# Performance work log

Measured on AMD Instinct MI355X. Metric: run time of the kernel, lower is better.

Reference implementation:

```python
import jax, jax.numpy as jnp
import numpy as np

NUM_HEADS = 8

def _ln(x, w, b, eps=1e-5):
    m = x.mean(-1, keepdims=True)
    v = ((x - m) ** 2).mean(-1, keepdims=True)
    return (x - m) / jnp.sqrt(v + eps) * w + b

def _conv3(x, w, b):
    y = jax.lax.conv_general_dilated(x, w, (1, 1), 'SAME',
                                     dimension_numbers=('NCHW', 'OIHW', 'NCHW'))
    return y + b[None, :, None, None]

def _pos_encoding(c, h, w, dtype):
    # first c//2 channels: x position in [0,1]; next c//2: y position
    px = jnp.broadcast_to(jnp.linspace(0, 1, w, dtype=dtype)[None, :], (h, w))
    py = jnp.broadcast_to(jnp.linspace(0, 1, h, dtype=dtype)[:, None], (h, w))
    pe = jnp.concatenate([jnp.broadcast_to(px, (c // 2, h, w)),
                          jnp.broadcast_to(py, (c // 2, h, w))], axis=0)
    return pe[None]  # [1,c,h,w]

def _pixel_shuffle(x, r=2):
    b, c4, h, w = x.shape
    c = c4 // (r * r)
    return x.reshape(b, c, r, r, h, w).transpose(0, 1, 4, 2, 5, 3).reshape(b, c, h * r, w * r)

def _forward(x, text_hidden, proj_w, proj_b, cf_w, cf_b,
             blk_qw, blk_qb, blk_kw, blk_kb, blk_vw, blk_vb,
             blk_ow, blk_ob, blk_ln1w, blk_ln1b, blk_ln2w, blk_ln2b,
             up_w, up_b, cl_w, cl_b):
    B = x.shape[0]
    # text projection: [B, L, text_dim] -> [B, L, C]
    tf = jnp.einsum('bld,cd->blc', text_hidden, proj_w) + proj_b
    feat = _conv3(x, cf_w, cf_b)  # [B, C, H, W]
    _, C, H, W = feat.shape
    L = tf.shape[1]
    hd = C // NUM_HEADS
    scale = hd ** (-0.5)
    pe = _pos_encoding(C, H, W, feat.dtype)

    def block(feat, p):
        qw, qb, kw, kb, vw, vb, ow, ob, l1w, l1b, l2w, l2b = p
        q = jnp.einsum('oi,bihw->bohw', qw, feat) + qb[None, :, None, None]
        q = q + pe * 0.05
        q_flat = q.reshape(B, C, H * W).transpose(0, 2, 1)  # [B, HW, C]
        q_norm = _ln(q_flat, l1w, l1b)
        qh = q_norm.reshape(B, H * W, NUM_HEADS, hd).transpose(0, 2, 1, 3)
        k = jnp.einsum('blc,oc->blo', tf, kw) + kb
        v = jnp.einsum('blc,oc->blo', tf, vw) + vb
        kn = _ln(k, l2w, l2b)
        kh = kn.reshape(B, L, NUM_HEADS, hd).transpose(0, 2, 1, 3)
        vh = v.reshape(B, L, NUM_HEADS, hd).transpose(0, 2, 1, 3)
        attn = jax.nn.softmax(jnp.einsum('bhnd,bhld->bhnl', qh, kh) * scale, axis=-1)
        out = jnp.einsum('bhnl,bhld->bhnd', attn, vh)          # [B, H8, HW, hd]
        out = out.transpose(0, 2, 1, 3).reshape(B, H * W, C)   # [B, HW, C]
        out = out.transpose(0, 2, 1).reshape(B, C, H, W)
        out = jnp.einsum('oi,bihw->bohw', ow, out) + ob[None, :, None, None]
        return out + feat, None

    blk_params = (blk_qw, blk_qb, blk_kw, blk_kb, blk_vw, blk_vb,
                  blk_ow, blk_ob, blk_ln1w, blk_ln1b, blk_ln2w, blk_ln2b)
    feat, _ = jax.lax.scan(block, feat, blk_params)

    for i in range(up_w.shape[0]):
        feat = jax.nn.relu(_pixel_shuffle(_conv3(feat, up_w[i], up_b[i]), 2))
    return _conv3(feat, cl_w, cl_b)


def setup_inputs() -> dict:
    key = jax.random.key(0)
    ks = jax.random.split(key, 20)
    B, H, W = 8, 64, 64
    C, D, L, NB = 64, 512, 77, 16
    s = 0.05
    inp = {
        'x': jax.random.normal(ks[0], (B, 3, H, W), jnp.float32),
        'text_hidden': jax.random.normal(ks[1], (B, L, D), jnp.float32),
        'proj_w': jax.random.normal(ks[2], (C, D), jnp.float32) * 0.01,
        'proj_b': jnp.zeros((C,), jnp.float32),
        'cf_w': jax.random.normal(ks[3], (C, 3, 3, 3), jnp.float32) * s,
        'cf_b': jnp.zeros((C,), jnp.float32),
        'blk_qw': jax.random.normal(ks[4], (NB, C, C), jnp.float32) * s,
        'blk_qb': jnp.zeros((NB, C), jnp.float32),
        'blk_kw': jax.random.normal(ks[5], (NB, C, C), jnp.float32) * 0.01,
        'blk_kb': jnp.zeros((NB, C), jnp.float32),
        'blk_vw': jax.random.normal(ks[6], (NB, C, C), jnp.float32) * 0.01,
        'blk_vb': jnp.zeros((NB, C), jnp.float32),
        'blk_ow': jax.random.normal(ks[7], (NB, C, C), jnp.float32) * s,
        'blk_ob': jnp.zeros((NB, C), jnp.float32),
        'blk_ln1w': jnp.ones((NB, C), jnp.float32),
        'blk_ln1b': jnp.zeros((NB, C), jnp.float32),
        'blk_ln2w': jnp.ones((NB, C), jnp.float32),
        'blk_ln2b': jnp.zeros((NB, C), jnp.float32),
        'up_w': jax.random.normal(ks[8], (2, C * 4, C, 3, 3), jnp.float32) * s,
        'up_b': jnp.zeros((2, C * 4), jnp.float32),
        'cl_w': jax.random.normal(ks[9], (3, C, 3, 3), jnp.float32) * s,
        'cl_b': jnp.zeros((3,), jnp.float32),
    }
    return inp


def reference(x, text_hidden, proj_w, proj_b, cf_w, cf_b,
              blk_qw, blk_qb, blk_kw, blk_kb, blk_vw, blk_vb,
              blk_ow, blk_ob, blk_ln1w, blk_ln1b, blk_ln2w, blk_ln2b,
              up_w, up_b, cl_w, cl_b):
    return _forward(x, text_hidden, proj_w, proj_b, cf_w, cf_b,
                    blk_qw, blk_qb, blk_kw, blk_kb, blk_vw, blk_vb,
                    blk_ow, blk_ob, blk_ln1w, blk_ln1b, blk_ln2w, blk_ln2b,
                    up_w, up_b, cl_w, cl_b)
```

## Files before the change

### kernel.cpp

```cpp
#include <hip/hip_runtime.h>
#include <math.h>

#define BATCH 8
#define C 64
#define NH 8
#define HD 8
#define LTXT 77
#define H0 64
#define W0 64
#define HW0 (H0*W0)

typedef __attribute__((ext_vector_type(8))) short bfrag;
typedef __attribute__((ext_vector_type(4))) float ffrag;
typedef __attribute__((ext_vector_type(8))) unsigned short us8;
typedef __attribute__((ext_vector_type(4))) unsigned short us4;
typedef __attribute__((ext_vector_type(2))) float f2;

#if defined(__has_builtin)
#if __has_builtin(__builtin_amdgcn_exp2f)
#define EXP2(x) __builtin_amdgcn_exp2f(x)
#else
#define EXP2(x) exp2f(x)
#endif
#else
#define EXP2(x) exp2f(x)
#endif

__device__ __forceinline__ unsigned short f2bf(float f) {
    unsigned u = __builtin_bit_cast(unsigned, f);
    u += 0x7fff + ((u >> 16) & 1);
    return (unsigned short)(u >> 16);
}

__global__ void text_proj_kernel(const float* __restrict__ th, const float* __restrict__ pw,
                                 const float* __restrict__ pb, float* __restrict__ tf) {
    __shared__ float sh[512];
    int bl = blockIdx.x;
    int c = threadIdx.x;
    const float* row = th + (size_t)bl * 512;
    for (int i = c; i < 512; i += 64) sh[i] = row[i];
    __syncthreads();
    const float* wrow = pw + c * 512;
    float acc = pb[c];
    for (int i = 0; i < 512; i += 4) {
        acc += sh[i] * wrow[i] + sh[i+1] * wrow[i+1] + sh[i+2] * wrow[i+2] + sh[i+3] * wrow[i+3];
    }
    tf[bl * 64 + c] = acc;
}

__global__ void __launch_bounds__(256)
prep_kernel(const float* __restrict__ x, const float* __restrict__ cf_w,
            const float* __restrict__ cf_b, float* __restrict__ feat,
            const float* __restrict__ up_w,
            unsigned short* __restrict__ PW1, unsigned short* __restrict__ PW2,
            const float* __restrict__ cl_w, unsigned short* __restrict__ PWF,
            const float* __restrict__ qw, const float* __restrict__ ow,
            unsigned short* __restrict__ PQ, unsigned short* __restrict__ PO) {
    int blk = blockIdx.x;
    if (blk < 8192) {
        int idx = blk * 256 + threadIdx.x;
        int wx = idx & 63;
        int h = (idx >> 6) & 63;
        int o = (idx >> 12) & 63;
        int b = idx >> 18;
        const float* wr = cf_w + o * 27;
        float acc = cf_b[o];
        for (int ci = 0; ci < 3; ci++) {
            for (int ky = 0; ky < 3; ky++) {
                int y = h + ky - 1;
                if ((unsigned)y >= 64u) continue;
                const float* xr = x + (((size_t)b * 3 + ci) * 64 + y) * 64;
                const float* wk = wr + ci * 9 + ky * 3;
                if (wx > 0) acc += xr[wx - 1] * wk[0];
                acc += xr[wx] * wk[1];
                if (wx < 63) acc += xr[wx + 1] * wk[2];
            }
        }
        feat[idx] = acc;
    } else if (blk < 8192 + 1152) {
        int e0 = blk - 8192;
        int st = e0 / 576;
        int e = (e0 % 576) * 256 + threadIdx.x;
        const float* w = up_w + (size_t)st * 147456;
        unsigned short* d = st ? PW2 : PW1;
        int j = e & 7, n = (e >> 3) & 255, q = (e >> 11) & 3, s = (e >> 13) & 1, t = e >> 14;
        int c = n & 63, g = n >> 6;
        int co = 4 * c + g, ci = 32 * s + 8 * q + j;
        d[e] = f2bf(w[co * 576 + ci * 9 + t]);
    } else if (blk < 8192 + 1152 + 36) {
        int e = (blk - 8192 - 1152) * 256 + threadIdx.x;
        int j = e & 7, n = (e >> 3) & 15, q = (e >> 7) & 3, s = (e >> 9) & 1, t = e >> 10;
        int ci = 32 * s + 8 * q + j;
        float v = (n < 3) ? cl_w[n * 576 + ci * 9 + t] : 0.f;
        PWF[e] = f2bf(v);
    } else {
        int e = (blk - 8192 - 1152 - 36) * 256 + threadIdx.x;
        int j = e & 7, n = (e >> 3) & 63, quad = (e >> 9) & 3, kt = (e >> 11) & 1, layer = e >> 12;
        int c = kt * 32 + quad * 8 + j;
        PQ[e] = f2bf(qw[layer * 4096 + n * 64 + c]);
        PO[e] = f2bf(ow[layer * 4096 + n * 64 + c]);
    }
}

__global__ void kv_all_kernel(const float* __restrict__ tf,
                              const float* __restrict__ kw, const float* __restrict__ kb,
                              const float* __restrict__ vw, const float* __restrict__ vb,
                              const float* __restrict__ l2w, const float* __restrict__ l2b,
                              float* __restrict__ kvbuf) {
    __shared__ float sh[64];
    int g = blockIdx.x;
    int bl = g % (BATCH * LTXT);
    int blk = g / (BATCH * LTXT);
    int o = threadIdx.x;
    sh[o] = tf[bl * 64 + o];
    __syncthreads();
    const float* kr = kw + blk * 4096 + o * 64;
    const float* vr = vw + blk * 4096 + o * 64;
    float ka = kb[blk * 64 + o], va = vb[blk * 64 + o];
    for (int c2 = 0; c2 < 64; c2++) {
        float t = sh[c2];
        ka += t * kr[c2];
        va += t * vr[c2];
    }
    float s = ka;
    for (int off = 32; off; off >>= 1) s += __shfl_xor(s, off, 64);
    float mean = s * (1.0f / 64.0f);
    float d = ka - mean;
    float s2 = d * d;
    for (int off = 32; off; off >>= 1) s2 += __shfl_xor(s2, off, 64);
    float rstd = rsqrtf(s2 * (1.0f / 64.0f) + 1e-5f);
    float kn = (d * rstd * l2w[blk * 64 + o] + l2b[blk * 64 + o]) * 0.51006973f;
    size_t base = ((size_t)blk * (BATCH * LTXT) + bl) * 128;
    int hd = o >> 3, ch = o & 7;
    kvbuf[base + hd * 16 + ch]     = kn;
    kvbuf[base + hd * 16 + 8 + ch] = va;
}

__global__ void __launch_bounds__(1024, 8)
attn_all_kernel(const float* __restrict__ feat,
                const float* __restrict__ kvbuf,
                const unsigned short* __restrict__ PQ, const unsigned short* __restrict__ PO,
                const float* __restrict__ qb_a, const float* __restrict__ ob_a,
                const float* __restrict__ l1w_a, const float* __restrict__ l1b_a,
                unsigned short* __restrict__ X1) {
    __shared__ __attribute__((aligned(16))) unsigned short sfb[64][72];
    __shared__ __attribute__((aligned(16))) unsigned short sob[64][72];
    __shared__ __attribute__((aligned(16))) float qf[64][68];
    __shared__ float so[64][64];
    __shared__ __attribute__((aligned(16))) float red[2][4][64];
    __shared__ float ss1[8][64];

    int b = blockIdx.x >> 6;
    int tile = blockIdx.x & 63;
    int n0 = tile << 6;
    int wv = __builtin_amdgcn_readfirstlane(threadIdx.x >> 6);
    int lane = threadIdx.x & 63;
    int p = lane;
    int quad = lane >> 4, n16 = lane & 15;
    int mt = wv >> 2, nt = wv & 3;
    int o0 = wv * 4;
    int h = wv >> 1, half = wv & 1;
    int a0 = h * 8;
    const float* fbase = feat + ((size_t)b << 18) + n0;

    float rres[4];
#pragma unroll
    for (int j = 0; j < 4; j++) rres[j] = fbase[(o0 + j) * HW0 + p];
    {
        us4 v;
#pragma unroll
        for (int j = 0; j < 4; j++) v[j] = f2bf(rres[j]);
        *(us4*)&sfb[p][o0] = v;
    }

    const float pxk = 0.05f / 63.0f;
    float py005 = (float)tile * pxk;
    __syncthreads();

#pragma unroll 1
    for (int layer = 0; layer < 16; layer++) {
        const float* qb = qb_a + layer * 64;
        const float* ob = ob_a + layer * 64;
        const float* l1w = l1w_a + layer * 64;
        const float* l1b = l1b_a + layer * 64;

        {
            bfrag af0 = *(const bfrag*)&sfb[mt * 16 + n16][quad * 8];
            bfrag af1 = *(const bfrag*)&sfb[mt * 16 + n16][32 + quad * 8];
            const unsigned short* bq = PQ + layer * 4096 + (size_t)((quad * 64) + nt * 16 + n16) * 8;
            bfrag bf0 = *(const bfrag*)bq;
            bfrag bf1 = *(const bfrag*)(bq + 2048);
            ffrag cc = (ffrag)0.f;
            cc = __builtin_amdgcn_mfma_f32_16x16x32_bf16(af0, bf0, cc, 0, 0, 0);
            cc = __builtin_amdgcn_mfma_f32_16x16x32_bf16(af1, bf1, cc, 0, 0, 0);
            int cch = nt * 16 + n16;
            float qbv = qb[cch];
            int p0 = mt * 16 + quad * 4;
            float pe0 = (nt < 2) ? (float)p0 * pxk : py005;
            float ped = (nt < 2) ? pxk : 0.f;
            float ov[4];
            ov[0] = cc[0] + qbv + pe0;
            ov[1] = cc[1] + qbv + pe0 + ped;
            ov[2] = cc[2] + qbv + pe0 + 2.f * ped;
            ov[3] = cc[3] + qbv + pe0 + 3.f * ped;
            float4 o4 = {ov[0], ov[1], ov[2], ov[3]};
            *(float4*)&qf[cch][p0] = o4;

            float sv[4], sq[4];
#pragma unroll
            for (int r = 0; r < 4; r++) {
                float s = ov[r], s2v = ov[r] * ov[r];
                s += __shfl_xor(s, 1);  s2v += __shfl_xor(s2v, 1);
                s += __shfl_xor(s, 2);  s2v += __shfl_xor(s2v, 2);
                s += __shfl_xor(s, 4);  s2v += __shfl_xor(s2v, 4);
                s += __shfl_xor(s, 8);  s2v += __shfl_xor(s2v, 8);
                sv[r] = s; sq[r] = s2v;
            }
            if (n16 == 0) {
                *(float4*)&red[0][nt][p0] = (float4){sv[0], sv[1], sv[2], sv[3]};
                *(float4*)&red[1][nt][p0] = (float4){sq[0], sq[1], sq[2], sq[3]};
            }
        }
        __syncthreads();

        {
            float ts = red[0][0][p] + red[0][1][p] + red[0][2][p] + red[0][3][p];
            float ts2 = red[1][0][p] + red[1][1][p] + red[1][2][p] + red[1][3][p];
            float mean = ts * (1.0f / 64.0f);
            float var = ts2 * (1.0f / 64.0f) - mean * mean;
            float rstd = rsqrtf(var + 1e-5f);

            f2 qv[4];
#pragma unroll
            for (int j = 0; j < 4; j++) {
                float qa  = (qf[a0 + 2 * j][p]     - mean) * rstd * l1w[a0 + 2 * j]     + l1b[a0 + 2 * j];
                float qbv = (qf[a0 + 2 * j + 1][p] - mean) * rstd * l1w[a0 + 2 * j + 1] + l1b[a0 + 2 * j + 1];
                qv[j][0] = qa;
                qv[j][1] = qbv;
            }
            const float* kvb = kvbuf + ((size_t)layer * BATCH * LTXT + (size_t)b * LTXT) * 128 + h * 16;
            int l0 = half ? 39 : 0;
            int l1 = half ? 77 : 39;
            float ssum = 0.f;
            f2 acc2[4] = {(f2)0.f, (f2)0.f, (f2)0.f, (f2)0.f};
            for (int l = l0; l < l1; l++) {
                const float4* r = (const float4*)(kvb + (size_t)l * 128);
                float4 k0 = r[0], k1 = r[1];
                f2 d2 = qv[0] * (f2){k0.x, k0.y};
                d2 += qv[1] * (f2){k0.z, k0.w};
                d2 += qv[2] * (f2){k1.x, k1.y};
                d2 += qv[3] * (f2){k1.z, k1.w};
                float e = EXP2(d2[0] + d2[1]);
                ssum += e;
                float4 v0 = r[2], v1 = r[3];
                f2 e2 = {e, e};
                acc2[0] += e2 * (f2){v0.x, v0.y};
                acc2[1] += e2 * (f2){v0.z, v0.w};
                acc2[2] += e2 * (f2){v1.x, v1.y};
                acc2[3] += e2 * (f2){v1.z, v1.w};
            }
            if (half) {
#pragma unroll
                for (int j = 0; j < 4; j++) {
                    so[a0 + 2 * j][p] = acc2[j][0];
                    so[a0 + 2 * j + 1][p] = acc2[j][1];
                }
                ss1[h][p] = ssum;
            }
            __syncthreads();
            if (!half) {
                float inv = 1.0f / (ssum + ss1[h][p]);
                us8 v;
#pragma unroll
                for (int j = 0; j < 4; j++) {
                    v[2*j]   = f2bf((acc2[j][0] + so[a0 + 2*j][p]) * inv);
                    v[2*j+1] = f2bf((acc2[j][1] + so[a0 + 2*j+1][p]) * inv);
                }
                *(us8*)&sob[p][a0] = v;
            }
        }
        __syncthreads();

        {
            bfrag af0 = *(const bfrag*)&sob[mt * 16 + n16][quad * 8];
            bfrag af1 = *(const bfrag*)&sob[mt * 16 + n16][32 + quad * 8];
            const unsigned short* bo = PO + layer * 4096 + (size_t)((quad * 64) + nt * 16 + n16) * 8;
            bfrag bf0 = *(const bfrag*)bo;
            bfrag bf1 = *(const bfrag*)(bo + 2048);
            ffrag cc = (ffrag)0.f;
            cc = __builtin_amdgcn_mfma_f32_16x16x32_bf16(af0, bf0, cc, 0, 0, 0);
            cc = __builtin_amdgcn_mfma_f32_16x16x32_bf16(af1, bf1, cc, 0, 0, 0);
            int cch = nt * 16 + n16;
            float obv = ob[cch];
            int p0 = mt * 16 + quad * 4;
            float4 o4;
            o4.x = cc[0] + obv; o4.y = cc[1] + obv; o4.z = cc[2] + obv; o4.w = cc[3] + obv;
            *(float4*)&qf[cch][p0] = o4;
        }
        __syncthreads();

        {
            us4 v;
#pragma unroll
            for (int j = 0; j < 4; j++) {
                rres[j] += qf[o0 + j][p];
                v[j] = f2bf(rres[j]);
            }
            *(us4*)&sfb[p][o0] = v;
        }
        __syncthreads();
    }

    us4 v;
#pragma unroll
    for (int j = 0; j < 4; j++) v[j] = f2bf(rres[j]);
    *(us4*)(X1 + ((size_t)(b * 4096 + n0 + p)) * 64 + o0) = v;
}

__global__ void __launch_bounds__(256)
upconv_mfma_kernel(const unsigned short* __restrict__ X, const unsigned short* __restrict__ Bp,
                   const float* __restrict__ bias, unsigned short* __restrict__ Y,
                   int Hin, int Win) {
    __shared__ __attribute__((aligned(16))) unsigned short sx[3 * 66 * 72];

    int y = blockIdx.y;
    int wv = threadIdx.x >> 6;
    int lane = threadIdx.x & 63;
    int q = lane >> 4, n16 = lane & 15;
    int m0 = blockIdx.x * 64;
    int hw = Hin * Win;
    int b = m0 / hw, rem = m0 % hw;
    int h = rem / Win, w0 = rem % Win;
    const unsigned short* Xb = X + (size_t)b * hw * 64;

    const us8 z8 = (us8)(unsigned short)0;
    for (int e = threadIdx.x; e < 1584; e += 256) {
        int ch8 = e & 7;
        int pxi = (e >> 3) % 66;
        int row = e / 528;
        int hh = h + row - 1, wp = w0 + pxi - 1;
        us8 v = z8;
        if ((unsigned)hh < (unsigned)Hin && (unsigned)wp < (unsigned)Win)
            v = *(const us8*)(Xb + ((size_t)hh * Win + wp) * 64 + ch8 * 8);
        *(us8*)&sx[row * 4752 + pxi * 72 + ch8 * 8] = v;
    }
    __syncthreads();

    ffrag acc[4][2];
#pragma unroll
    for (int i = 0; i < 4; i++)
#pragma unroll
        for (int j2 = 0; j2 < 2; j2++) acc[i][j2] = (ffrag)0.f;

    int npb = y * 128 + wv * 32;

    for (int t = 0; t < 9; t++) {
        int dy = t / 3, dx = t % 3;
        bfrag af[4][2];
#pragma unroll
        for (int mt = 0; mt < 4; mt++) {
            const unsigned short* sp = &sx[dy * 4752 + (mt * 16 + n16 + dx) * 72 + q * 8];
            af[mt][0] = *(const bfrag*)sp;
            af[mt][1] = *(const bfrag*)(sp + 32);
        }
#pragma unroll
        for (int s = 0; s < 2; s++) {
#pragma unroll
            for (int nt = 0; nt < 2; nt++) {
                bfrag bf = *(const bfrag*)(Bp + (size_t)((((t * 2 + s) * 4 + q) * 256) + npb + nt * 16 + n16) * 8);
#pragma unroll
                for (int mt = 0; mt < 4; mt++)
                    acc[mt][nt] = __builtin_amdgcn_mfma_f32_16x16x32_bf16(af[mt][s], bf, acc[mt][nt], 0, 0, 0);
            }
        }
    }

    int g = y * 2 + (wv >> 1);
    int r1 = y, r2 = wv >> 1;
    int cbase = (wv & 1) * 32;
    float bv[2];
#pragma unroll
    for (int nt = 0; nt < 2; nt++) bv[nt] = bias[4 * (cbase + nt * 16 + n16) + g];
    int Wo = Win * 2;
    unsigned short* Yb = Y + ((size_t)b * Hin * 2 * Wo + (size_t)(2 * h + r1) * Wo + r2) * 64;
#pragma unroll
    for (int mt = 0; mt < 4; mt++) {
#pragma unroll
        for (int r = 0; r < 4; r++) {
            int m = mt * 16 + q * 4 + r;
            unsigned short* dst = Yb + (size_t)(2 * (w0 + m)) * 64;
#pragma unroll
            for (int nt = 0; nt < 2; nt++) {
                float v = acc[mt][nt][r] + bv[nt];
                v = fmaxf(v, 0.f);
                dst[cbase + nt * 16 + n16] = f2bf(v);
            }
        }
    }
}

__global__ void __launch_bounds__(256)
final_mfma_kernel(const unsigned short* __restrict__ X, const unsigned short* __restrict__ Bp,
                  const float* __restrict__ bias, float* __restrict__ out) {
    __shared__ __attribute__((aligned(16))) unsigned short sx[6 * 66 * 72];

    int t0 = blockIdx.x;
    int wseg = t0 & 3;
    int rg = (t0 >> 2) & 63;
    int b = t0 >> 8;
    int y0 = rg * 4, w0 = wseg * 64;
    int wv = threadIdx.x >> 6, lane = threadIdx.x & 63;
    int q = lane >> 4, n16 = lane & 15;
    const unsigned short* Xb = X + (size_t)b * 65536 * 64;

    const us8 z8 = (us8)(unsigned short)0;
    for (int e = threadIdx.x; e < 3168; e += 256) {
        int ch8 = e & 7;
        int pxi = (e >> 3) % 66;
        int row = e / 528;
        int hh = y0 - 1 + row, wp = w0 - 1 + pxi;
        us8 v = z8;
        if ((unsigned)hh < 256u && (unsigned)wp < 256u)
            v = *(const us8*)(Xb + ((size_t)hh * 256 + wp) * 64 + ch8 * 8);
        *(us8*)&sx[row * 4752 + pxi * 72 + ch8 * 8] = v;
    }
    __syncthreads();

    ffrag acc[4];
#pragma unroll
    for (int i = 0; i < 4; i++) acc[i] = (ffrag)0.f;

    for (int t = 0; t < 9; t++) {
        int dy = t / 3, dx = t % 3;
        bfrag af[4][2];
#pragma unroll
        for (int mt = 0; mt < 4; mt++) {
            const unsigned short* sp = &sx[(wv + dy) * 4752 + (mt * 16 + n16 + dx) * 72 + q * 8];
            af[mt][0] = *(const bfrag*)sp;
            af[mt][1] = *(const bfrag*)(sp + 32);
        }
#pragma unroll
        for (int s = 0; s < 2; s++) {
            bfrag bf = *(const bfrag*)(Bp + (size_t)((((t * 2 + s) * 4 + q) * 16) + n16) * 8);
#pragma unroll
            for (int mt = 0; mt < 4; mt++)
                acc[mt] = __builtin_amdgcn_mfma_f32_16x16x32_bf16(af[mt][s], bf, acc[mt], 0, 0, 0);
        }
    }

    if (n16 < 3) {
        float bj = bias[n16];
        float* ob = out + (((size_t)b * 3 + n16) * 256 + (y0 + wv)) * 256;
#pragma unroll
        for (int mt = 0; mt < 4; mt++)
#pragma unroll
            for (int r = 0; r < 4; r++)
                ob[w0 + mt * 16 + q * 4 + r] = acc[mt][r] + bj;
    }
}

extern "C" void kernel_launch(void* const* d_in, const int* in_sizes, int n_in,
                              void* d_out, int out_size, void* d_ws, size_t ws_size,
                              hipStream_t stream) {
    const float* x      = (const float*)d_in[0];
    const float* th     = (const float*)d_in[1];
    const float* proj_w = (const float*)d_in[2];
    const float* proj_b = (const float*)d_in[3];
    const float* cf_w   = (const float*)d_in[4];
    const float* cf_b   = (const float*)d_in[5];
    const float* qw     = (const float*)d_in[6];
    const float* qb     = (const float*)d_in[7];
    const float* kw     = (const float*)d_in[8];
    const float* kb     = (const float*)d_in[9];
    const float* vw     = (const float*)d_in[10];
    const float* vb     = (const float*)d_in[11];
    const float* ow     = (const float*)d_in[12];
    const float* ob     = (const float*)d_in[13];
    const float* l1w    = (const float*)d_in[14];
    const float* l1b    = (const float*)d_in[15];
    const float* l2w    = (const float*)d_in[16];
    const float* l2b    = (const float*)d_in[17];
    const float* up_w   = (const float*)d_in[18];
    const float* up_b   = (const float*)d_in[19];
    const float* cl_w   = (const float*)d_in[20];
    const float* cl_b   = (const float*)d_in[21];

    float* ws   = (float*)d_ws;
    float* feat = ws;
    float* tf   = feat + 2097152;
    float* kvbuf = tf + 39424;
    unsigned short* X1  = (unsigned short*)(kvbuf + 1261568);
    unsigned short* X2  = X1 + 2097152;
    unsigned short* X3  = X2 + 8388608;
    unsigned short* PW1 = X3 + 33554432;
    unsigned short* PW2 = PW1 + 147456;
    unsigned short* PWF = PW2 + 147456;
    unsigned short* PQ  = PWF + 9216;
    unsigned short* PO  = PQ + 65536;

    hipLaunchKernelGGL(prep_kernel, dim3(8192 + 1152 + 36 + 256), dim3(256), 0, stream,
                       x, cf_w, cf_b, feat, up_w, PW1, PW2, cl_w, PWF, qw, ow, PQ, PO);
    hipLaunchKernelGGL(text_proj_kernel, dim3(BATCH * LTXT), dim3(64), 0, stream,
                       th, proj_w, proj_b, tf);
    hipLaunchKernelGGL(kv_all_kernel, dim3(16 * BATCH * LTXT), dim3(64), 0, stream,
                       tf, kw, kb, vw, vb, l2w, l2b, kvbuf);

    hipLaunchKernelGGL(attn_all_kernel, dim3(BATCH * (HW0 / 64)), dim3(1024), 0, stream,
                       feat, kvbuf, PQ, PO, qb, ob, l1w, l1b, X1);

    hipLaunchKernelGGL(upconv_mfma_kernel, dim3(BATCH * 64 * 64 / 64, 2), dim3(256), 0, stream,
                       X1, PW1, up_b, X2, 64, 64);
    hipLaunchKernelGGL(upconv_mfma_kernel, dim3(BATCH * 128 * 128 / 64, 2), dim3(256), 0, stream,
                       X2, PW2, up_b + 256, X3, 128, 128);
    hipLaunchKernelGGL(final_mfma_kernel, dim3(BATCH * 64 * 4), dim3(256), 0, stream,
                       X3, PWF, cl_b, (float*)d_out);
}
```

Baseline: 549.7 us.

## Halve attention tile to 32 pixels and merge upconv y-split into one block

The attention kernel now handles 32 pixels per block with 512 threads. Each wave owns one head and splits the 77 text tokens across its two half-waves, combining the partial softmax sums with cross-lane shuffles instead of shared memory and an extra barrier. This doubles the grid and cuts LDS use, which should improve occupancy and remove a sync per layer. The upconv kernel drops the two-way grid.y split and uses 512 threads per block, so each block covers all output channels and the halo tile is loaded only once per block.

```diff
diff --git a/kernel.cpp b/kernel.cpp
--- a/kernel.cpp
+++ b/kernel.cpp
@@ -136,45 +136,47 @@
     kvbuf[base + hd * 16 + 8 + ch] = va;
 }
 
-__global__ void __launch_bounds__(1024, 8)
+__global__ void __launch_bounds__(512, 8)
 attn_all_kernel(const float* __restrict__ feat,
                 const float* __restrict__ kvbuf,
                 const unsigned short* __restrict__ PQ, const unsigned short* __restrict__ PO,
                 const float* __restrict__ qb_a, const float* __restrict__ ob_a,
                 const float* __restrict__ l1w_a, const float* __restrict__ l1b_a,
                 unsigned short* __restrict__ X1) {
-    __shared__ __attribute__((aligned(16))) unsigned short sfb[64][72];
-    __shared__ __attribute__((aligned(16))) unsigned short sob[64][72];
-    __shared__ __attribute__((aligned(16))) float qf[64][68];
-    __shared__ float so[64][64];
-    __shared__ __attribute__((aligned(16))) float red[2][4][64];
-    __shared__ float ss1[8][64];
-
-    int b = blockIdx.x >> 6;
-    int tile = blockIdx.x & 63;
-    int n0 = tile << 6;
+    __shared__ __attribute__((aligned(16))) unsigned short sfb[32][72];
+    __shared__ __attribute__((aligned(16))) unsigned short sob[32][72];
+    __shared__ __attribute__((aligned(16))) float qf[64][36];
+    __shared__ __attribute__((aligned(16))) float red[2][4][32];
+
+    int b = blockIdx.x >> 7;
+    int tile = blockIdx.x & 127;
+    int n0 = tile << 5;
     int wv = __builtin_amdgcn_readfirstlane(threadIdx.x >> 6);
     int lane = threadIdx.x & 63;
-    int p = lane;
+    int px = lane & 31;
+    int th = lane >> 5;
     int quad = lane >> 4, n16 = lane & 15;
     int mt = wv >> 2, nt = wv & 3;
-    int o0 = wv * 4;
-    int h = wv >> 1, half = wv & 1;
+    int cch = nt * 16 + n16;
+    int p0 = mt * 16 + quad * 4;
+    int h = wv;
     int a0 = h * 8;
+    int co = wv * 8 + th * 4;
     const float* fbase = feat + ((size_t)b << 18) + n0;
 
     float rres[4];
 #pragma unroll
-    for (int j = 0; j < 4; j++) rres[j] = fbase[(o0 + j) * HW0 + p];
+    for (int j = 0; j < 4; j++) rres[j] = fbase[(co + j) * HW0 + px];
     {
         us4 v;
 #pragma unroll
         for (int j = 0; j < 4; j++) v[j] = f2bf(rres[j]);
-        *(us4*)&sfb[p][o0] = v;
+        *(us4*)&sfb[px][co] = v;
     }
 
     const float pxk = 0.05f / 63.0f;
-    float py005 = (float)tile * pxk;
+    float pex_base = (float)((tile & 1) * 32) * pxk;
+    float pey = (float)(tile >> 1) * pxk;
     __syncthreads();
 
 #pragma unroll 1
@@ -187,16 +189,14 @@
         {
             bfrag af0 = *(const bfrag*)&sfb[mt * 16 + n16][quad * 8];
             bfrag af1 = *(const bfrag*)&sfb[mt * 16 + n16][32 + quad * 8];
-            const unsigned short* bq = PQ + layer * 4096 + (size_t)((quad * 64) + nt * 16 + n16) * 8;
+            const unsigned short* bq = PQ + layer * 4096 + (size_t)((quad * 64) + cch) * 8;
             bfrag bf0 = *(const bfrag*)bq;
             bfrag bf1 = *(const bfrag*)(bq + 2048);
             ffrag cc = (ffrag)0.f;
             cc = __builtin_amdgcn_mfma_f32_16x16x32_bf16(af0, bf0, cc, 0, 0, 0);
             cc = __builtin_amdgcn_mfma_f32_16x16x32_bf16(af1, bf1, cc, 0, 0, 0);
-            int cch = nt * 16 + n16;
             float qbv = qb[cch];
-            int p0 = mt * 16 + quad * 4;
-            float pe0 = (nt < 2) ? (float)p0 * pxk : py005;
+            float pe0 = (nt < 2) ? pex_base + (float)p0 * pxk : pey;
             float ped = (nt < 2) ? pxk : 0.f;
             float ov[4];
             ov[0] = cc[0] + qbv + pe0;
@@ -224,8 +224,8 @@
         __syncthreads();
 
         {
-            float ts = red[0][0][p] + red[0][1][p] + red[0][2][p] + red[0][3][p];
-            float ts2 = red[1][0][p] + red[1][1][p] + red[1][2][p] + red[1][3][p];
+            float ts = red[0][0][px] + red[0][1][px] + red[0][2][px] + red[0][3][px];
+            float ts2 = red[1][0][px] + red[1][1][px] + red[1][2][px] + red[1][3][px];
             float mean = ts * (1.0f / 64.0f);
             float var = ts2 * (1.0f / 64.0f) - mean * mean;
             float rstd = rsqrtf(var + 1e-5f);
@@ -233,50 +233,63 @@
             f2 qv[4];
 #pragma unroll
             for (int j = 0; j < 4; j++) {
-                float qa  = (qf[a0 + 2 * j][p]     - mean) * rstd * l1w[a0 + 2 * j]     + l1b[a0 + 2 * j];
-                float qbv = (qf[a0 + 2 * j + 1][p] - mean) * rstd * l1w[a0 + 2 * j + 1] + l1b[a0 + 2 * j + 1];
+                float qa  = (qf[a0 + 2 * j][px]     - mean) * rstd * l1w[a0 + 2 * j]     + l1b[a0 + 2 * j];
+                float qbv = (qf[a0 + 2 * j + 1][px] - mean) * rstd * l1w[a0 + 2 * j + 1] + l1b[a0 + 2 * j + 1];
                 qv[j][0] = qa;
                 qv[j][1] = qbv;
             }
-            const float* kvb = kvbuf + ((size_t)layer * BATCH * LTXT + (size_t)b * LTXT) * 128 + h * 16;
-            int l0 = half ? 39 : 0;
-            int l1 = half ? 77 : 39;
+            const float* kvb = kvbuf + ((size_t)layer * BATCH * LTXT + (size_t)b * LTXT) * 128 + h * 16
+                             + (size_t)(th * 39) * 128;
             float ssum = 0.f;
             f2 acc2[4] = {(f2)0.f, (f2)0.f, (f2)0.f, (f2)0.f};
-            for (int l = l0; l < l1; l++) {
-                const float4* r = (const float4*)(kvb + (size_t)l * 128);
-                float4 k0 = r[0], k1 = r[1];
+            for (int i = 0; i < 38; i++) {
+                const float4* r = (const float4*)(kvb + (size_t)i * 128);
+                float4 k0 = r[0], k1 = r[1], v0 = r[2], v1 = r[3];
                 f2 d2 = qv[0] * (f2){k0.x, k0.y};
                 d2 += qv[1] * (f2){k0.z, k0.w};
                 d2 += qv[2] * (f2){k1.x, k1.y};
                 d2 += qv[3] * (f2){k1.z, k1.w};
                 float e = EXP2(d2[0] + d2[1]);
                 ssum += e;
-                float4 v0 = r[2], v1 = r[3];
                 f2 e2 = {e, e};
                 acc2[0] += e2 * (f2){v0.x, v0.y};
                 acc2[1] += e2 * (f2){v0.z, v0.w};
                 acc2[2] += e2 * (f2){v1.x, v1.y};
                 acc2[3] += e2 * (f2){v1.z, v1.w};
             }
-            if (half) {
+            {
+                size_t ioff = (size_t)(th ? 37 : 38) * 128;
+                const float4* r = (const float4*)(kvb + ioff);
+                float4 k0 = r[0], k1 = r[1], v0 = r[2], v1 = r[3];
+                f2 d2 = qv[0] * (f2){k0.x, k0.y};
+                d2 += qv[1] * (f2){k0.z, k0.w};
+                d2 += qv[2] * (f2){k1.x, k1.y};
+                d2 += qv[3] * (f2){k1.z, k1.w};
+                float e = EXP2(d2[0] + d2[1]);
+                if (th) e = 0.f;
+                ssum += e;
+                f2 e2 = {e, e};
+                acc2[0] += e2 * (f2){v0.x, v0.y};
+                acc2[1] += e2 * (f2){v0.z, v0.w};
+                acc2[2] += e2 * (f2){v1.x, v1.y};
+                acc2[3] += e2 * (f2){v1.z, v1.w};
+            }
+            float stot = ssum + __shfl_xor(ssum, 32, 64);
+            f2 atot[4];
+#pragma unroll
+            for (int j = 0; j < 4; j++) {
+                atot[j][0] = acc2[j][0] + __shfl_xor(acc2[j][0], 32, 64);
+                atot[j][1] = acc2[j][1] + __shfl_xor(acc2[j][1], 32, 64);
+            }
+            if (!th) {
+                float inv = 1.0f / stot;
+                us8 v;
 #pragma unroll
                 for (int j = 0; j < 4; j++) {
-                    so[a0 + 2 * j][p] = acc2[j][0];
-                    so[a0 + 2 * j + 1][p] = acc2[j][1];
+                    v[2*j]   = f2bf(atot[j][0] * inv);
+                    v[2*j+1] = f2bf(atot[j][1] * inv);
                 }
-                ss1[h][p] = ssum;
-            }
-            __syncthreads();
-            if (!half) {
-                float inv = 1.0f / (ssum + ss1[h][p]);
-                us8 v;
-#pragma unroll
-                for (int j = 0; j < 4; j++) {
-                    v[2*j]   = f2bf((acc2[j][0] + so[a0 + 2*j][p]) * inv);
-                    v[2*j+1] = f2bf((acc2[j][1] + so[a0 + 2*j+1][p]) * inv);
-                }
-                *(us8*)&sob[p][a0] = v;
+                *(us8*)&sob[px][a0] = v;
             }
         }
         __syncthreads();
@@ -284,15 +297,13 @@
         {
             bfrag af0 = *(const bfrag*)&sob[mt * 16 + n16][quad * 8];
             bfrag af1 = *(const bfrag*)&sob[mt * 16 + n16][32 + quad * 8];
-            const unsigned short* bo = PO + layer * 4096 + (size_t)((quad * 64) + nt * 16 + n16) * 8;
+            const unsigned short* bo = PO + layer * 4096 + (size_t)((quad * 64) + cch) * 8;
             bfrag bf0 = *(const bfrag*)bo;
             bfrag bf1 = *(const bfrag*)(bo + 2048);
             ffrag cc = (ffrag)0.f;
             cc = __builtin_amdgcn_mfma_f32_16x16x32_bf16(af0, bf0, cc, 0, 0, 0);
             cc = __builtin_amdgcn_mfma_f32_16x16x32_bf16(af1, bf1, cc, 0, 0, 0);
-            int cch = nt * 16 + n16;
             float obv = ob[cch];
-            int p0 = mt * 16 + quad * 4;
             float4 o4;
             o4.x = cc[0] + obv; o4.y = cc[1] + obv; o4.z = cc[2] + obv; o4.w = cc[3] + obv;
             *(float4*)&qf[cch][p0] = o4;
@@ -303,10 +314,10 @@
             us4 v;
 #pragma unroll
             for (int j = 0; j < 4; j++) {
-                rres[j] += qf[o0 + j][p];
+                rres[j] += qf[co + j][px];
                 v[j] = f2bf(rres[j]);
             }
-            *(us4*)&sfb[p][o0] = v;
+            *(us4*)&sfb[px][co] = v;
         }
         __syncthreads();
     }
@@ -314,16 +325,15 @@
     us4 v;
 #pragma unroll
     for (int j = 0; j < 4; j++) v[j] = f2bf(rres[j]);
-    *(us4*)(X1 + ((size_t)(b * 4096 + n0 + p)) * 64 + o0) = v;
-}
-
-__global__ void __launch_bounds__(256)
+    *(us4*)(X1 + ((size_t)(b * 4096 + n0 + px)) * 64 + co) = v;
+}
+
+__global__ void __launch_bounds__(512)
 upconv_mfma_kernel(const unsigned short* __restrict__ X, const unsigned short* __restrict__ Bp,
                    const float* __restrict__ bias, unsigned short* __restrict__ Y,
                    int Hin, int Win) {
     __shared__ __attribute__((aligned(16))) unsigned short sx[3 * 66 * 72];
 
-    int y = blockIdx.y;
     int wv = threadIdx.x >> 6;
     int lane = threadIdx.x & 63;
     int q = lane >> 4, n16 = lane & 15;
@@ -334,7 +344,7 @@
     const unsigned short* Xb = X + (size_t)b * hw * 64;
 
     const us8 z8 = (us8)(unsigned short)0;
-    for (int e = threadIdx.x; e < 1584; e += 256) {
+    for (int e = threadIdx.x; e < 1584; e += 512) {
         int ch8 = e & 7;
         int pxi = (e >> 3) % 66;
         int row = e / 528;
@@ -352,7 +362,7 @@
 #pragma unroll
         for (int j2 = 0; j2 < 2; j2++) acc[i][j2] = (ffrag)0.f;
 
-    int npb = y * 128 + wv * 32;
+    int npb = wv * 32;
 
     for (int t = 0; t < 9; t++) {
         int dy = t / 3, dx = t % 3;
@@ -375,8 +385,8 @@
         }
     }
 
-    int g = y * 2 + (wv >> 1);
-    int r1 = y, r2 = wv >> 1;
+    int g = wv >> 1;
+    int r1 = wv >> 2, r2 = (wv >> 1) & 1;
     int cbase = (wv & 1) * 32;
     float bv[2];
 #pragma unroll
@@ -505,12 +515,12 @@
     hipLaunchKernelGGL(kv_all_kernel, dim3(16 * BATCH * LTXT), dim3(64), 0, stream,
                        tf, kw, kb, vw, vb, l2w, l2b, kvbuf);
 
-    hipLaunchKernelGGL(attn_all_kernel, dim3(BATCH * (HW0 / 64)), dim3(1024), 0, stream,
+    hipLaunchKernelGGL(attn_all_kernel, dim3(BATCH * (HW0 / 32)), dim3(512), 0, stream,
                        feat, kvbuf, PQ, PO, qb, ob, l1w, l1b, X1);
 
-    hipLaunchKernelGGL(upconv_mfma_kernel, dim3(BATCH * 64 * 64 / 64, 2), dim3(256), 0, stream,
+    hipLaunchKernelGGL(upconv_mfma_kernel, dim3(BATCH * 64 * 64 / 64), dim3(512), 0, stream,
                        X1, PW1, up_b, X2, 64, 64);
-    hipLaunchKernelGGL(upconv_mfma_kernel, dim3(BATCH * 128 * 128 / 64, 2), dim3(256), 0, stream,
+    hipLaunchKernelGGL(upconv_mfma_kernel, dim3(BATCH * 128 * 128 / 64), dim3(512), 0, stream,
                        X2, PW2, up_b + 256, X3, 128, 128);
     hipLaunchKernelGGL(final_mfma_kernel, dim3(BATCH * 64 * 4), dim3(256), 0, stream,
                        X3, PWF, cl_b, (float*)d_out);
```

Measured after the change: 914.7 us. 66.4% more time.

## Store K/V in bf16, stage per-layer K/V in LDS, merge upconv channel halves

Applied to the files above, without the earlier changes.

The K/V buffer is now written as bf16, which halves its size. Each layer, the attention kernel copies the K/V for its batch into shared memory and computes QK dot products with bf16 fdot2 when that builtin exists. The upconv kernel now runs 512 threads per block and covers both output-channel halves, so the input halo tile is loaded once instead of twice. The cost is lower precision on K, V and Q, and a per-layer LDS fill with no barrier before the reads, which may be a race.

```diff
diff --git a/kernel.cpp b/kernel.cpp
--- a/kernel.cpp
+++ b/kernel.cpp
@@ -22,6 +22,10 @@
 #else
 #define EXP2(x) exp2f(x)
 #endif
+#if __has_builtin(__builtin_amdgcn_fdot2_f32_bf16)
+#define USE_DOT2 1
+typedef __bf16 bf2v __attribute__((ext_vector_type(2)));
+#endif
 #else
 #define EXP2(x) exp2f(x)
 #endif
@@ -30,6 +34,13 @@
     unsigned u = __builtin_bit_cast(unsigned, f);
     u += 0x7fff + ((u >> 16) & 1);
     return (unsigned short)(u >> 16);
+}
+
+__device__ __forceinline__ f2 bfp2f2(unsigned w) {
+    f2 r;
+    r[0] = __builtin_bit_cast(float, w << 16);
+    r[1] = __builtin_bit_cast(float, w & 0xffff0000u);
+    return r;
 }
 
 __global__ void text_proj_kernel(const float* __restrict__ th, const float* __restrict__ pw,
@@ -106,7 +117,7 @@
                               const float* __restrict__ kw, const float* __restrict__ kb,
                               const float* __restrict__ vw, const float* __restrict__ vb,
                               const float* __restrict__ l2w, const float* __restrict__ l2b,
-                              float* __restrict__ kvbuf) {
+                              unsigned short* __restrict__ kvi) {
     __shared__ float sh[64];
     int g = blockIdx.x;
     int bl = g % (BATCH * LTXT);
@@ -132,13 +143,13 @@
     float kn = (d * rstd * l2w[blk * 64 + o] + l2b[blk * 64 + o]) * 0.51006973f;
     size_t base = ((size_t)blk * (BATCH * LTXT) + bl) * 128;
     int hd = o >> 3, ch = o & 7;
-    kvbuf[base + hd * 16 + ch]     = kn;
-    kvbuf[base + hd * 16 + 8 + ch] = va;
+    kvi[base + hd * 16 + ch]     = f2bf(kn);
+    kvi[base + hd * 16 + 8 + ch] = f2bf(va);
 }
 
 __global__ void __launch_bounds__(1024, 8)
 attn_all_kernel(const float* __restrict__ feat,
-                const float* __restrict__ kvbuf,
+                const unsigned short* __restrict__ kvi,
                 const unsigned short* __restrict__ PQ, const unsigned short* __restrict__ PO,
                 const float* __restrict__ qb_a, const float* __restrict__ ob_a,
                 const float* __restrict__ l1w_a, const float* __restrict__ l1b_a,
@@ -149,6 +160,7 @@
     __shared__ float so[64][64];
     __shared__ __attribute__((aligned(16))) float red[2][4][64];
     __shared__ float ss1[8][64];
+    __shared__ __attribute__((aligned(16))) unsigned short skv[LTXT * 128];
 
     int b = blockIdx.x >> 6;
     int tile = blockIdx.x & 63;
@@ -183,6 +195,16 @@
         const float* ob = ob_a + layer * 64;
         const float* l1w = l1w_a + layer * 64;
         const float* l1b = l1b_a + layer * 64;
+
+        {
+            const us8* gk = (const us8*)(kvi + (((size_t)layer * BATCH + b) * LTXT) * 128);
+            us8* sk = (us8*)skv;
+            int e = threadIdx.x;
+            us8 c0 = gk[e];
+            us8 c1 = (e + 1024 < 1232) ? gk[e + 1024] : c0;
+            sk[e] = c0;
+            if (e + 1024 < 1232) sk[e + 1024] = c1;
+        }
 
         {
             bfrag af0 = *(const bfrag*)&sfb[mt * 16 + n16][quad * 8];
@@ -230,6 +252,22 @@
             float var = ts2 * (1.0f / 64.0f) - mean * mean;
             float rstd = rsqrtf(var + 1e-5f);
 
+#if defined(USE_DOT2)
+            unsigned qp[4];
+#pragma unroll
+            for (int j = 0; j < 4; j++) {
+                float qa  = (qf[a0 + 2 * j][p]     - mean) * rstd * l1w[a0 + 2 * j]     + l1b[a0 + 2 * j];
+                float qbv = (qf[a0 + 2 * j + 1][p] - mean) * rstd * l1w[a0 + 2 * j + 1] + l1b[a0 + 2 * j + 1];
+                qp[j] = (unsigned)f2bf(qa) | ((unsigned)f2bf(qbv) << 16);
+            }
+#define QKDOT(kk) ({ \
+    float dd = 0.f; \
+    dd = __builtin_amdgcn_fdot2_f32_bf16(__builtin_bit_cast(bf2v, (kk).x), __builtin_bit_cast(bf2v, qp[0]), dd, false); \
+    dd = __builtin_amdgcn_fdot2_f32_bf16(__builtin_bit_cast(bf2v, (kk).y), __builtin_bit_cast(bf2v, qp[1]), dd, false); \
+    dd = __builtin_amdgcn_fdot2_f32_bf16(__builtin_bit_cast(bf2v, (kk).z), __builtin_bit_cast(bf2v, qp[2]), dd, false); \
+    dd = __builtin_amdgcn_fdot2_f32_bf16(__builtin_bit_cast(bf2v, (kk).w), __builtin_bit_cast(bf2v, qp[3]), dd, false); \
+    dd; })
+#else
             f2 qv[4];
 #pragma unroll
             for (int j = 0; j < 4; j++) {
@@ -238,27 +276,53 @@
                 qv[j][0] = qa;
                 qv[j][1] = qbv;
             }
-            const float* kvb = kvbuf + ((size_t)layer * BATCH * LTXT + (size_t)b * LTXT) * 128 + h * 16;
+#define QKDOT(kk) ({ \
+    f2 d2 = qv[0] * bfp2f2((kk).x); \
+    d2 += qv[1] * bfp2f2((kk).y); \
+    d2 += qv[2] * bfp2f2((kk).z); \
+    d2 += qv[3] * bfp2f2((kk).w); \
+    d2[0] + d2[1]; })
+#endif
+            const unsigned short* kvl = &skv[h * 16];
             int l0 = half ? 39 : 0;
             int l1 = half ? 77 : 39;
             float ssum = 0.f;
             f2 acc2[4] = {(f2)0.f, (f2)0.f, (f2)0.f, (f2)0.f};
-            for (int l = l0; l < l1; l++) {
-                const float4* r = (const float4*)(kvb + (size_t)l * 128);
-                float4 k0 = r[0], k1 = r[1];
-                f2 d2 = qv[0] * (f2){k0.x, k0.y};
-                d2 += qv[1] * (f2){k0.z, k0.w};
-                d2 += qv[2] * (f2){k1.x, k1.y};
-                d2 += qv[3] * (f2){k1.z, k1.w};
-                float e = EXP2(d2[0] + d2[1]);
+            int l = l0;
+            for (; l + 2 <= l1; l += 2) {
+                uint4 ka = *(const uint4*)(kvl + (size_t)l * 128);
+                uint4 va = *(const uint4*)(kvl + (size_t)l * 128 + 8);
+                uint4 kb2 = *(const uint4*)(kvl + (size_t)(l + 1) * 128);
+                uint4 vb2 = *(const uint4*)(kvl + (size_t)(l + 1) * 128 + 8);
+
+                float ea = EXP2(QKDOT(ka));
+                ssum += ea;
+                f2 ea2 = {ea, ea};
+                acc2[0] += ea2 * bfp2f2(va.x);
+                acc2[1] += ea2 * bfp2f2(va.y);
+                acc2[2] += ea2 * bfp2f2(va.z);
+                acc2[3] += ea2 * bfp2f2(va.w);
+
+                float eb = EXP2(QKDOT(kb2));
+                ssum += eb;
+                f2 eb2 = {eb, eb};
+                acc2[0] += eb2 * bfp2f2(vb2.x);
+                acc2[1] += eb2 * bfp2f2(vb2.y);
+                acc2[2] += eb2 * bfp2f2(vb2.z);
+                acc2[3] += eb2 * bfp2f2(vb2.w);
+            }
+            if (l < l1) {
+                uint4 kc = *(const uint4*)(kvl + (size_t)l * 128);
+                uint4 vc = *(const uint4*)(kvl + (size_t)l * 128 + 8);
+                float e = EXP2(QKDOT(kc));
                 ssum += e;
-                float4 v0 = r[2], v1 = r[3];
                 f2 e2 = {e, e};
-                acc2[0] += e2 * (f2){v0.x, v0.y};
-                acc2[1] += e2 * (f2){v0.z, v0.w};
-                acc2[2] += e2 * (f2){v1.x, v1.y};
-                acc2[3] += e2 * (f2){v1.z, v1.w};
-            }
+                acc2[0] += e2 * bfp2f2(vc.x);
+                acc2[1] += e2 * bfp2f2(vc.y);
+                acc2[2] += e2 * bfp2f2(vc.z);
+                acc2[3] += e2 * bfp2f2(vc.w);
+            }
+#undef QKDOT
             if (half) {
 #pragma unroll
                 for (int j = 0; j < 4; j++) {
@@ -317,13 +381,12 @@
     *(us4*)(X1 + ((size_t)(b * 4096 + n0 + p)) * 64 + o0) = v;
 }
 
-__global__ void __launch_bounds__(256)
+__global__ void __launch_bounds__(512)
 upconv_mfma_kernel(const unsigned short* __restrict__ X, const unsigned short* __restrict__ Bp,
                    const float* __restrict__ bias, unsigned short* __restrict__ Y,
                    int Hin, int Win) {
     __shared__ __attribute__((aligned(16))) unsigned short sx[3 * 66 * 72];
 
-    int y = blockIdx.y;
     int wv = threadIdx.x >> 6;
     int lane = threadIdx.x & 63;
     int q = lane >> 4, n16 = lane & 15;
@@ -334,7 +397,7 @@
     const unsigned short* Xb = X + (size_t)b * hw * 64;
 
     const us8 z8 = (us8)(unsigned short)0;
-    for (int e = threadIdx.x; e < 1584; e += 256) {
+    for (int e = threadIdx.x; e < 1584; e += 512) {
         int ch8 = e & 7;
         int pxi = (e >> 3) % 66;
         int row = e / 528;
@@ -352,7 +415,7 @@
 #pragma unroll
         for (int j2 = 0; j2 < 2; j2++) acc[i][j2] = (ffrag)0.f;
 
-    int npb = y * 128 + wv * 32;
+    int npb = wv * 32;
 
     for (int t = 0; t < 9; t++) {
         int dy = t / 3, dx = t % 3;
@@ -375,8 +438,8 @@
         }
     }
 
-    int g = y * 2 + (wv >> 1);
-    int r1 = y, r2 = wv >> 1;
+    int g = wv >> 1;
+    int r1 = wv >> 2, r2 = (wv >> 1) & 1;
     int cbase = (wv & 1) * 32;
     float bv[2];
 #pragma unroll
@@ -488,8 +551,8 @@
     float* ws   = (float*)d_ws;
     float* feat = ws;
     float* tf   = feat + 2097152;
-    float* kvbuf = tf + 39424;
-    unsigned short* X1  = (unsigned short*)(kvbuf + 1261568);
+    unsigned short* kvi = (unsigned short*)(tf + 39424);
+    unsigned short* X1  = kvi + 1261568;
     unsigned short* X2  = X1 + 2097152;
     unsigned short* X3  = X2 + 8388608;
     unsigned short* PW1 = X3 + 33554432;
@@ -503,14 +566,14 @@
     hipLaunchKernelGGL(text_proj_kernel, dim3(BATCH * LTXT), dim3(64), 0, stream,
                        th, proj_w, proj_b, tf);
     hipLaunchKernelGGL(kv_all_kernel, dim3(16 * BATCH * LTXT), dim3(64), 0, stream,
-                       tf, kw, kb, vw, vb, l2w, l2b, kvbuf);
+                       tf, kw, kb, vw, vb, l2w, l2b, kvi);
 
     hipLaunchKernelGGL(attn_all_kernel, dim3(BATCH * (HW0 / 64)), dim3(1024), 0, stream,
-                       feat, kvbuf, PQ, PO, qb, ob, l1w, l1b, X1);
-
-    hipLaunchKernelGGL(upconv_mfma_kernel, dim3(BATCH * 64 * 64 / 64, 2), dim3(256), 0, stream,
+                       feat, kvi, PQ, PO, qb, ob, l1w, l1b, X1);
+
+    hipLaunchKernelGGL(upconv_mfma_kernel, dim3(BATCH * 64 * 64 / 64), dim3(512), 0, stream,
                        X1, PW1, up_b, X2, 64, 64);
-    hipLaunchKernelGGL(upconv_mfma_kernel, dim3(BATCH * 128 * 128 / 64, 2), dim3(256), 0, stream,
+    hipLaunchKernelGGL(upconv_mfma_kernel, dim3(BATCH * 128 * 128 / 64), dim3(512), 0, stream,
                        X2, PW2, up_b + 256, X3, 128, 128);
     hipLaunchKernelGGL(final_mfma_kernel, dim3(BATCH * 64 * 4), dim3(256), 0, stream,
                        X3, PWF, cl_b, (float*)d_out);
```

Result: no change. 542.1 us (-1.4%).
